# Kernel optimization log

Measured on AMD Instinct MI355X. Metric: run time of the kernel, lower is better.

The kernel has to match this reference:

```python
import jax, jax.numpy as jnp
import numpy as np

N_DRUGS = 4096
W_DIM = 512
N_SUB = 10
N_EDGES = 131072


def setup_inputs() -> dict:
    key = jax.random.key(0)
    k1, k2, k3, k4 = jax.random.split(key, 4)
    z_drug = jax.random.normal(k1, (N_DRUGS, W_DIM), dtype=jnp.float32)
    # glorot-ish init for weights
    global_weight = jax.random.normal(k2, (W_DIM, W_DIM), dtype=jnp.float32) * (2.0 / (2 * W_DIM)) ** 0.5
    local_diag = jax.random.normal(k3, (N_SUB, W_DIM), dtype=jnp.float32) * (2.0 / (W_DIM + 1)) ** 0.5
    batch_edges = jax.random.randint(k4, (2, N_EDGES), 0, N_DRUGS, dtype=jnp.int64)
    return {
        "z_drug": z_drug,
        "global_weight": global_weight,
        "local_diag": local_diag,
        "batch_edges": batch_edges,
        "edge_sub_type_idx": 2,
    }


def reference(z_drug, global_weight, local_diag, batch_edges, edge_sub_type_idx):
    # edge_type == 'drug_drug': z1 = z2 = z_drug
    row_embed = z_drug[batch_edges[0]]            # [B, D]
    col_embed = z_drug[batch_edges[1]]            # [B, D]
    d = local_diag[edge_sub_type_idx]             # [D] diagonal of local weight matrix
    # row @ diag(d) @ W @ diag(d) == ((row * d) @ W) * d
    p = ((row_embed * d) @ global_weight) * d     # [B, D]
    # diagonal(p @ col^T) == rowwise dot product
    score = jnp.sum(p * col_embed, axis=-1)       # [B]
    return jax.nn.sigmoid(score)
```

## Files before the change

kernel.cpp:

```cpp
#include <hip/hip_runtime.h>
#include <cstdint>

#define ND 4096
#define D  512

typedef __bf16 bf16x8 __attribute__((ext_vector_type(8)));
typedef float floatx4 __attribute__((ext_vector_type(4)));
typedef unsigned short ushort8 __attribute__((ext_vector_type(8)));

__device__ __forceinline__ float bf2f(unsigned short b) {
    return __uint_as_float(((unsigned int)b) << 16);
}
__device__ __forceinline__ unsigned short f2bf(float f) {
    unsigned int u = __float_as_uint(f);
    u += 0x7fffu + ((u >> 16) & 1u);
    return (unsigned short)(u >> 16);
}
__device__ __forceinline__ float lo16(unsigned int u) { return __uint_as_float(u << 16); }
__device__ __forceinline__ float hi16(unsigned int u) { return __uint_as_float(u & 0xffff0000u); }

__device__ __forceinline__ void gll16(const void* g, void* l) {
    __builtin_amdgcn_global_load_lds((const __attribute__((address_space(1))) unsigned int*)g,
                                     (__attribute__((address_space(3))) unsigned int*)l,
                                     16, 0, 0);
}

__device__ __forceinline__ int2 detect_flags(const unsigned short* z, const int* ed) {
    int lane = threadIdx.x & 63;
    unsigned short u = z[lane];
    int e = (u >> 7) & 0xFF;
    unsigned long long b0 = __ballot(e >= 96 && e <= 160);
    unsigned long long b1 = __ballot(ed[2 * lane + 1] == 0);
    int2 f;
    f.x = (__popcll(b0) >= 56) ? 1 : 0;
    f.y = (__popcll(b1) >= 56) ? 1 : 0;
    return f;
}

__global__ __launch_bounds__(256) void prep_kernel(const void* __restrict__ Wv,
                                                   const void* __restrict__ ldv,
                                                   const int* __restrict__ sub,
                                                   unsigned short* __restrict__ Mt,
                                                   unsigned short* __restrict__ zb,
                                                   const void* __restrict__ z,
                                                   const int* __restrict__ ed) {
    __shared__ float xp[64][65];
    int2 f = detect_flags((const unsigned short*)z, ed);
    int bf = f.x;

    if (blockIdx.x >= 64) {
        if (bf) return;
        int idx = (int)(blockIdx.x - 64) * 256 + threadIdx.x;
        const float* zf = (const float*)z;
#pragma unroll
        for (int it = 0; it < 4; it++) {
            int base = (it * 65536 + idx) * 8;
            float4 f0 = *(const float4*)(zf + base);
            float4 f1 = *(const float4*)(zf + base + 4);
            union { ushort8 u; uint4 v; } cv;
            cv.u[0] = f2bf(f0.x); cv.u[1] = f2bf(f0.y);
            cv.u[2] = f2bf(f0.z); cv.u[3] = f2bf(f0.w);
            cv.u[4] = f2bf(f1.x); cv.u[5] = f2bf(f1.y);
            cv.u[6] = f2bf(f1.z); cv.u[7] = f2bf(f1.w);
            *(uint4*)(zb + base) = cv.v;
        }
        return;
    }

    int su = sub[0];
    if ((unsigned)su > 9u) su = 2;
    int k0 = (blockIdx.x & 7) * 64, n0 = (blockIdx.x >> 3) * 64;
    int j = threadIdx.x & 63, w = threadIdx.x >> 6;
#pragma unroll
    for (int r = 0; r < 16; r++) {
        int k = k0 + w * 16 + r;
        float v = bf ? bf2f(((const unsigned short*)Wv)[k * D + n0 + j])
                     : ((const float*)Wv)[k * D + n0 + j];
        xp[w * 16 + r][j] = v;
    }
    __syncthreads();
    int k = k0 + j;
    float dk = bf ? bf2f(((const unsigned short*)ldv)[su * D + k])
                  : ((const float*)ldv)[su * D + k];
#pragma unroll
    for (int r = 0; r < 16; r++) {
        int n = n0 + w * 16 + r;
        float dn = bf ? bf2f(((const unsigned short*)ldv)[su * D + n])
                      : ((const float*)ldv)[su * D + n];
        Mt[n * D + k] = f2bf(xp[j][w * 16 + r] * dk * dn);
    }
}

__global__ __launch_bounds__(256) void gemm_kernel(const void* __restrict__ z,
                                                   const unsigned short* __restrict__ zb,
                                                   const unsigned short* __restrict__ Mt,
                                                   unsigned short* __restrict__ Y,
                                                   const int* __restrict__ ed) {
    __shared__ __bf16 As[2][8 * 512];
    __shared__ __bf16 Bs[2][8 * 512];
    int2 f = detect_flags((const unsigned short*)z, ed);
    const unsigned short* A = f.x ? (const unsigned short*)z : zb;

    int tid = threadIdx.x;
    int w = tid >> 6, lane = tid & 63;
    int rl = lane & 15, quad = lane >> 4;
    int bx = blockIdx.x;
    int xcd = bx & 7, idx = bx >> 3;
    int tm = (xcd * 8 + (idx & 7)) * 64;
    int tn = (idx >> 3) * 64;
    int wm = (w >> 1) * 32, wn = (w & 1) * 32;

    const unsigned short* Ap = A + (tm + lane) * D;
    const unsigned short* Bp = Mt + (tn + lane) * D;

    floatx4 acc[2][2] = {};

    auto stage = [&](int buf, int kk) {
#pragma unroll
        for (int t = 0; t < 2; t++) {
            int kb = w * 2 + t;
            gll16(Bp + kk + kb * 8, &Bs[buf][kb * 512]);
            gll16(Ap + kk + kb * 8, &As[buf][kb * 512]);
        }
    };
    auto compute = [&](int buf) {
#pragma unroll
        for (int kc = 0; kc < 64; kc += 32) {
            int kb0 = kc >> 3;
            bf16x8 a0 = *(const bf16x8*)(&As[buf][(kb0 + quad) * 512 + (wm + rl) * 8]);
            bf16x8 a1 = *(const bf16x8*)(&As[buf][(kb0 + quad) * 512 + (wm + 16 + rl) * 8]);
            bf16x8 b0 = *(const bf16x8*)(&Bs[buf][(kb0 + quad) * 512 + (wn + rl) * 8]);
            bf16x8 b1 = *(const bf16x8*)(&Bs[buf][(kb0 + quad) * 512 + (wn + 16 + rl) * 8]);
            acc[0][0] = __builtin_amdgcn_mfma_f32_16x16x32_bf16(a0, b0, acc[0][0], 0, 0, 0);
            acc[0][1] = __builtin_amdgcn_mfma_f32_16x16x32_bf16(a0, b1, acc[0][1], 0, 0, 0);
            acc[1][0] = __builtin_amdgcn_mfma_f32_16x16x32_bf16(a1, b0, acc[1][0], 0, 0, 0);
            acc[1][1] = __builtin_amdgcn_mfma_f32_16x16x32_bf16(a1, b1, acc[1][1], 0, 0, 0);
        }
    };

    stage(0, 0);
    __syncthreads();
#pragma unroll
    for (int kt = 1; kt < 8; kt++) {
        int cur = (kt - 1) & 1;
        stage(cur ^ 1, kt * 64);
        compute(cur);
        __syncthreads();
    }
    compute(1);

#pragma unroll
    for (int j = 0; j < 2; j++) {
        int col = tn + wn + j * 16 + rl;
#pragma unroll
        for (int i = 0; i < 2; i++) {
            int rbase = tm + wm + i * 16 + quad * 4;
#pragma unroll
            for (int r = 0; r < 4; r++)
                Y[(rbase + r) * D + col] = f2bf(acc[i][j][r]);
        }
    }
}

template <bool I64>
__device__ void edge_slice_body(const unsigned short* __restrict__ Y,
                                const unsigned short* __restrict__ zc,
                                const int* __restrict__ ed,
                                float* __restrict__ partial, int E) {
    int slice = blockIdx.x & 7;
    int egrp  = blockIdx.x >> 3;
    int lane = threadIdx.x & 63;
    int w = threadIdx.x >> 6;
    int sub8 = lane >> 3;
    int l = lane & 7;
    int col = slice * 64 + l * 8;
    int e0 = egrp * 256 + w * 8 + sub8;

    if (egrp * 256 + 255 < E) {
        int r[8], c[8];
#pragma unroll
        for (int i = 0; i < 8; i++) {
            int e = e0 + i * 32;
            if constexpr (I64) { r[i] = ed[2 * e] & (ND - 1); c[i] = ed[2 * (E + e)] & (ND - 1); }
            else               { r[i] = ed[e] & (ND - 1);     c[i] = ed[E + e] & (ND - 1); }
        }
        float s[8];
#pragma unroll
        for (int i = 0; i < 8; i++) {
            uint4 yu = *(const uint4*)(Y + r[i] * D + col);
            uint4 zu = *(const uint4*)(zc + c[i] * D + col);
            s[i]  = lo16(yu.x) * lo16(zu.x) + hi16(yu.x) * hi16(zu.x);
            s[i] += lo16(yu.y) * lo16(zu.y) + hi16(yu.y) * hi16(zu.y);
            s[i] += lo16(yu.z) * lo16(zu.z) + hi16(yu.z) * hi16(zu.z);
            s[i] += lo16(yu.w) * lo16(zu.w) + hi16(yu.w) * hi16(zu.w);
        }
#pragma unroll
        for (int i = 0; i < 8; i++) {
            s[i] += __shfl_xor(s[i], 1, 64);
            s[i] += __shfl_xor(s[i], 2, 64);
            s[i] += __shfl_xor(s[i], 4, 64);
            if (l == 0)
                partial[slice * E + e0 + i * 32] = s[i];
        }
    } else {
#pragma unroll
        for (int i = 0; i < 8; i++) {
            int e = e0 + i * 32;
            if (e >= E) continue;
            int r, c;
            if constexpr (I64) { r = ed[2 * e]; c = ed[2 * (E + e)]; }
            else               { r = ed[e];     c = ed[E + e]; }
            r &= ND - 1; c &= ND - 1;
            uint4 yu = *(const uint4*)(Y + r * D + col);
            uint4 zu = *(const uint4*)(zc + c * D + col);
            float s;
            s  = lo16(yu.x) * lo16(zu.x) + hi16(yu.x) * hi16(zu.x);
            s += lo16(yu.y) * lo16(zu.y) + hi16(yu.y) * hi16(zu.y);
            s += lo16(yu.z) * lo16(zu.z) + hi16(yu.z) * hi16(zu.z);
            s += lo16(yu.w) * lo16(zu.w) + hi16(yu.w) * hi16(zu.w);
            s += __shfl_xor(s, 1, 64);
            s += __shfl_xor(s, 2, 64);
            s += __shfl_xor(s, 4, 64);
            if (l == 0)
                partial[slice * E + e] = s;
        }
    }
}

__global__ __launch_bounds__(256) void edge_slice(const unsigned short* __restrict__ Y,
                                                  const void* __restrict__ z,
                                                  const unsigned short* __restrict__ zb,
                                                  const int* __restrict__ ed,
                                                  float* __restrict__ partial, int E) {
    int2 f = detect_flags((const unsigned short*)z, ed);
    const unsigned short* zc = f.x ? (const unsigned short*)z : zb;
    if (f.y) edge_slice_body<true >(Y, zc, ed, partial, E);
    else     edge_slice_body<false>(Y, zc, ed, partial, E);
}

__global__ __launch_bounds__(256) void finish_kernel(const float* __restrict__ partial,
                                                     const unsigned short* __restrict__ zdet,
                                                     const int* __restrict__ eddet,
                                                     void* __restrict__ out, int E) {
    int2 f = detect_flags(zdet, eddet);
    int e = blockIdx.x * 256 + threadIdx.x;
    if (e >= E) return;
    float t = 0.f;
#pragma unroll
    for (int s = 0; s < 8; s++)
        t += partial[s * E + e];
    if (!(t > -1e30f && t < 1e30f)) t = 0.0f;
    float sig = 1.0f / (1.0f + __expf(-t));
    if (f.x) ((unsigned short*)out)[e] = f2bf(sig);
    else     ((float*)out)[e] = sig;
}

extern "C" void kernel_launch(void* const* d_in, const int* in_sizes, int n_in,
                              void* d_out, int out_size, void* d_ws, size_t ws_size,
                              hipStream_t stream) {
    const void* z     = d_in[0];
    const void* W     = d_in[1];
    const void* ldiag = d_in[2];
    const int* edges  = (const int*)d_in[3];
    const int* sub    = (const int*)d_in[4];
    int E = out_size;

    char* ws = (char*)d_ws;
    unsigned short* Y  = (unsigned short*)ws;
    unsigned short* Mt = (unsigned short*)(ws + 4194304);
    float* partial     = (float*)(ws + 4194304 + 524288);
    unsigned short* zb = (unsigned short*)(ws + 4194304 + 524288 + 4194304);

    prep_kernel<<<320, 256, 0, stream>>>(W, ldiag, sub, Mt, zb, z, edges);
    gemm_kernel<<<512, 256, 0, stream>>>(z, zb, Mt, Y, edges);
    int sblocks = ((E + 255) / 256) * 8;
    edge_slice<<<sblocks, 256, 0, stream>>>(Y, z, zb, edges, partial, E);
    finish_kernel<<<(E + 255) / 256, 256, 0, stream>>>(partial, (const unsigned short*)z,
                                                       edges, d_out, E);
}
```

Measured before the change: 104.1 us.

## Fuse finish into edge kernel via last-block counter and halve column slices

Removes the separate finish kernel. The last of the four slice blocks for each edge group, detected through an atomic counter, sums the partials and writes the sigmoid output. Slices drop from 8 to 4, so each lane loads 32 bytes per row and the index loads and partial writes are roughly halved. In exchange it adds threadfence/atomic synchronisation and counter zeroing in the prep kernel, and launches fewer blocks.

```diff
diff --git a/kernel.cpp b/kernel.cpp
--- a/kernel.cpp
+++ b/kernel.cpp
@@ -43,8 +43,12 @@
                                                    unsigned short* __restrict__ Mt,
                                                    unsigned short* __restrict__ zb,
                                                    const void* __restrict__ z,
-                                                   const int* __restrict__ ed) {
+                                                   const int* __restrict__ ed,
+                                                   int* __restrict__ cnt, int ngrp) {
     __shared__ float xp[64][65];
+    int gi = (int)blockIdx.x * 256 + threadIdx.x;
+    if (gi < ngrp) cnt[gi] = 0;
+
     int2 f = detect_flags((const unsigned short*)z, ed);
     int bf = f.x;
 
@@ -166,14 +170,16 @@
 __device__ void edge_slice_body(const unsigned short* __restrict__ Y,
                                 const unsigned short* __restrict__ zc,
                                 const int* __restrict__ ed,
-                                float* __restrict__ partial, int E) {
-    int slice = blockIdx.x & 7;
-    int egrp  = blockIdx.x >> 3;
+                                float* __restrict__ partial,
+                                int* __restrict__ cnt,
+                                void* __restrict__ out, int bfout, int E) {
+    int slice = blockIdx.x & 3;
+    int egrp  = blockIdx.x >> 2;
     int lane = threadIdx.x & 63;
     int w = threadIdx.x >> 6;
     int sub8 = lane >> 3;
     int l = lane & 7;
-    int col = slice * 64 + l * 8;
+    int col = slice * 128 + l * 16;
     int e0 = egrp * 256 + w * 8 + sub8;
 
     if (egrp * 256 + 255 < E) {
@@ -187,12 +193,18 @@
         float s[8];
 #pragma unroll
         for (int i = 0; i < 8; i++) {
-            uint4 yu = *(const uint4*)(Y + r[i] * D + col);
-            uint4 zu = *(const uint4*)(zc + c[i] * D + col);
-            s[i]  = lo16(yu.x) * lo16(zu.x) + hi16(yu.x) * hi16(zu.x);
-            s[i] += lo16(yu.y) * lo16(zu.y) + hi16(yu.y) * hi16(zu.y);
-            s[i] += lo16(yu.z) * lo16(zu.z) + hi16(yu.z) * hi16(zu.z);
-            s[i] += lo16(yu.w) * lo16(zu.w) + hi16(yu.w) * hi16(zu.w);
+            const uint4* yp = (const uint4*)(Y + r[i] * D + col);
+            const uint4* zp = (const uint4*)(zc + c[i] * D + col);
+            uint4 y0 = yp[0], y1 = yp[1];
+            uint4 z0 = zp[0], z1 = zp[1];
+            s[i]  = lo16(y0.x) * lo16(z0.x) + hi16(y0.x) * hi16(z0.x);
+            s[i] += lo16(y0.y) * lo16(z0.y) + hi16(y0.y) * hi16(z0.y);
+            s[i] += lo16(y0.z) * lo16(z0.z) + hi16(y0.z) * hi16(z0.z);
+            s[i] += lo16(y0.w) * lo16(z0.w) + hi16(y0.w) * hi16(z0.w);
+            s[i] += lo16(y1.x) * lo16(z1.x) + hi16(y1.x) * hi16(z1.x);
+            s[i] += lo16(y1.y) * lo16(z1.y) + hi16(y1.y) * hi16(z1.y);
+            s[i] += lo16(y1.z) * lo16(z1.z) + hi16(y1.z) * hi16(z1.z);
+            s[i] += lo16(y1.w) * lo16(z1.w) + hi16(y1.w) * hi16(z1.w);
         }
 #pragma unroll
         for (int i = 0; i < 8; i++) {
@@ -211,13 +223,19 @@
             if constexpr (I64) { r = ed[2 * e]; c = ed[2 * (E + e)]; }
             else               { r = ed[e];     c = ed[E + e]; }
             r &= ND - 1; c &= ND - 1;
-            uint4 yu = *(const uint4*)(Y + r * D + col);
-            uint4 zu = *(const uint4*)(zc + c * D + col);
+            const uint4* yp = (const uint4*)(Y + r * D + col);
+            const uint4* zp = (const uint4*)(zc + c * D + col);
+            uint4 y0 = yp[0], y1 = yp[1];
+            uint4 z0 = zp[0], z1 = zp[1];
             float s;
-            s  = lo16(yu.x) * lo16(zu.x) + hi16(yu.x) * hi16(zu.x);
-            s += lo16(yu.y) * lo16(zu.y) + hi16(yu.y) * hi16(zu.y);
-            s += lo16(yu.z) * lo16(zu.z) + hi16(yu.z) * hi16(zu.z);
-            s += lo16(yu.w) * lo16(zu.w) + hi16(yu.w) * hi16(zu.w);
+            s  = lo16(y0.x) * lo16(z0.x) + hi16(y0.x) * hi16(z0.x);
+            s += lo16(y0.y) * lo16(z0.y) + hi16(y0.y) * hi16(z0.y);
+            s += lo16(y0.z) * lo16(z0.z) + hi16(y0.z) * hi16(z0.z);
+            s += lo16(y0.w) * lo16(z0.w) + hi16(y0.w) * hi16(z0.w);
+            s += lo16(y1.x) * lo16(z1.x) + hi16(y1.x) * hi16(z1.x);
+            s += lo16(y1.y) * lo16(z1.y) + hi16(y1.y) * hi16(z1.y);
+            s += lo16(y1.z) * lo16(z1.z) + hi16(y1.z) * hi16(z1.z);
+            s += lo16(y1.w) * lo16(z1.w) + hi16(y1.w) * hi16(z1.w);
             s += __shfl_xor(s, 1, 64);
             s += __shfl_xor(s, 2, 64);
             s += __shfl_xor(s, 4, 64);
@@ -225,34 +243,35 @@
                 partial[slice * E + e] = s;
         }
     }
+
+    __threadfence();
+    __syncthreads();
+    __shared__ int lastFlag;
+    if (threadIdx.x == 0)
+        lastFlag = (atomicAdd(&cnt[egrp], 1) == 3);
+    __syncthreads();
+    if (!lastFlag) return;
+    __threadfence();
+    int e = egrp * 256 + threadIdx.x;
+    if (e >= E) return;
+    float t = partial[e] + partial[E + e] + partial[2 * E + e] + partial[3 * E + e];
+    if (!(t > -1e30f && t < 1e30f)) t = 0.0f;
+    float sig = 1.0f / (1.0f + __expf(-t));
+    if (bfout) ((unsigned short*)out)[e] = f2bf(sig);
+    else       ((float*)out)[e] = sig;
 }
 
 __global__ __launch_bounds__(256) void edge_slice(const unsigned short* __restrict__ Y,
                                                   const void* __restrict__ z,
                                                   const unsigned short* __restrict__ zb,
                                                   const int* __restrict__ ed,
-                                                  float* __restrict__ partial, int E) {
+                                                  float* __restrict__ partial,
+                                                  int* __restrict__ cnt,
+                                                  void* __restrict__ out, int E) {
     int2 f = detect_flags((const unsigned short*)z, ed);
     const unsigned short* zc = f.x ? (const unsigned short*)z : zb;
-    if (f.y) edge_slice_body<true >(Y, zc, ed, partial, E);
-    else     edge_slice_body<false>(Y, zc, ed, partial, E);
-}
-
-__global__ __launch_bounds__(256) void finish_kernel(const float* __restrict__ partial,
-                                                     const unsigned short* __restrict__ zdet,
-                                                     const int* __restrict__ eddet,
-                                                     void* __restrict__ out, int E) {
-    int2 f = detect_flags(zdet, eddet);
-    int e = blockIdx.x * 256 + threadIdx.x;
-    if (e >= E) return;
-    float t = 0.f;
-#pragma unroll
-    for (int s = 0; s < 8; s++)
-        t += partial[s * E + e];
-    if (!(t > -1e30f && t < 1e30f)) t = 0.0f;
-    float sig = 1.0f / (1.0f + __expf(-t));
-    if (f.x) ((unsigned short*)out)[e] = f2bf(sig);
-    else     ((float*)out)[e] = sig;
+    if (f.y) edge_slice_body<true >(Y, zc, ed, partial, cnt, out, f.x, E);
+    else     edge_slice_body<false>(Y, zc, ed, partial, cnt, out, f.x, E);
 }
 
 extern "C" void kernel_launch(void* const* d_in, const int* in_sizes, int n_in,
@@ -264,17 +283,18 @@
     const int* edges  = (const int*)d_in[3];
     const int* sub    = (const int*)d_in[4];
     int E = out_size;
+    int ngrp = (E + 255) / 256;
 
     char* ws = (char*)d_ws;
     unsigned short* Y  = (unsigned short*)ws;
     unsigned short* Mt = (unsigned short*)(ws + 4194304);
-    float* partial     = (float*)(ws + 4194304 + 524288);
-    unsigned short* zb = (unsigned short*)(ws + 4194304 + 524288 + 4194304);
-
-    prep_kernel<<<320, 256, 0, stream>>>(W, ldiag, sub, Mt, zb, z, edges);
+    size_t poff = 4194304 + 524288;
+    float* partial     = (float*)(ws + poff);
+    size_t zoff = poff + (((size_t)4 * E * 4 + 255) & ~(size_t)255);
+    unsigned short* zb = (unsigned short*)(ws + zoff);
+    int* cnt           = (int*)(ws + zoff + 4194304);
+
+    prep_kernel<<<320, 256, 0, stream>>>(W, ldiag, sub, Mt, zb, z, edges, cnt, ngrp);
     gemm_kernel<<<512, 256, 0, stream>>>(z, zb, Mt, Y, edges);
-    int sblocks = ((E + 255) / 256) * 8;
-    edge_slice<<<sblocks, 256, 0, stream>>>(Y, z, zb, edges, partial, E);
-    finish_kernel<<<(E + 255) / 256, 256, 0, stream>>>(partial, (const unsigned short*)z,
-                                                       edges, d_out, E);
-}
+    edge_slice<<<ngrp * 4, 256, 0, stream>>>(Y, z, zb, edges, partial, cnt, d_out, E);
+}
```

Result: slower. 342.2 us (+228.7%).
